# Performance work log

Hardware: AMD Instinct MI355X
Metric: run time of the kernel (lower is better)

## Reference

```python
import jax, jax.numpy as jnp
import numpy as np

N, IN_DIM, HID, EMB, PROJ = 12000, 256, 256, 128, 128
LN_EPS = 1e-5

def _layer_norm(h, gamma, beta):
    mu = jnp.mean(h, axis=-1, keepdims=True)
    var = jnp.mean(jnp.square(h - mu), axis=-1, keepdims=True)
    return (h - mu) * jax.lax.rsqrt(var + LN_EPS) * gamma + beta

def setup_inputs() -> dict:
    key = jax.random.key(0)
    ks = jax.random.split(key, 16)
    def lin(k, fan_in, fan_out):
        bound = 1.0 / np.sqrt(fan_in)
        kw, kb = jax.random.split(k)
        W = jax.random.uniform(kw, (fan_in, fan_out), jnp.float32, -bound, bound)
        b = jax.random.uniform(kb, (fan_out,), jnp.float32, -bound, bound)
        return W, b
    W1, b1 = lin(ks[0], IN_DIM, HID)
    W2, b2 = lin(ks[1], HID, HID)
    W3, b3 = lin(ks[2], HID, EMB)
    Wp1, bp1 = lin(ks[3], EMB, PROJ)
    Wp2, bp2 = lin(ks[4], PROJ, PROJ)
    x = jax.random.normal(ks[5], (N, IN_DIM), jnp.float32)
    # dense adjacency (row-stochastic-ish, scaled so aggregated values stay sane)
    adj = jax.random.uniform(ks[6], (N, N), jnp.float32) / N
    return {
        "x": x, "adj": adj,
        "W1": W1, "b1": b1, "g1": jnp.ones((HID,), jnp.float32), "be1": jnp.zeros((HID,), jnp.float32),
        "W2": W2, "b2": b2, "g2": jnp.ones((HID,), jnp.float32), "be2": jnp.zeros((HID,), jnp.float32),
        "W3": W3, "b3": b3,
        "Wp1": Wp1, "bp1": bp1, "Wp2": Wp2, "bp2": bp2,
    }

def reference(x, adj, W1, b1, g1, be1, W2, b2, g2, be2, W3, b3, Wp1, bp1, Wp2, bp2):
    # eval mode: dropout and dropout_adj are identity
    # layer 1: GCNConv_dense = A @ (x W + b); residual = x (in_dim == hidden_dim)
    h = adj @ (x @ W1 + b1)
    h = _layer_norm(h + x, g1, be1)
    h = jax.nn.relu(h)
    h_prev = h
    # layer 2
    h2 = adj @ (h @ W2 + b2)
    h2 = _layer_norm(h2 + h_prev, g2, be2)
    h2 = jax.nn.relu(h2)
    # final conv -> embedding (no norm/relu/residual)
    embedding = adj @ (h2 @ W3 + b3)
    # proj head: Linear -> ReLU -> Linear
    z = jax.nn.relu(embedding @ Wp1 + bp1) @ Wp2 + bp2
    return (z, embedding)
```

## Files before the change

### kernel.cpp

```cpp
#include <hip/hip_runtime.h>

typedef unsigned short u16;
typedef unsigned int u32;
typedef __attribute__((ext_vector_type(8))) short bf16x8;
typedef __attribute__((ext_vector_type(8))) u16 u16x8;
typedef __attribute__((ext_vector_type(4))) u16 u16x4;
typedef __attribute__((ext_vector_type(4))) float f32x4;

#define DEV static __device__ __forceinline__

DEV u16 f2bf(float f) {
    union { float f; u32 u; } v; v.f = f;
    u32 r = v.u + 0x7FFFu + ((v.u >> 16) & 1u);
    return (u16)(r >> 16);
}

DEV int swzc(int r, int c) { return c ^ ((r >> 1) & 3); }

DEV void gload_lds16(const void* g, void* l) {
    __builtin_amdgcn_global_load_lds((const __attribute__((address_space(1))) void*)g,
                                     (__attribute__((address_space(3))) void*)l, 16, 0, 0);
}

template<int BN, int MINW, bool AF32, bool BF32, bool DUMPA, int BIAS, bool RELU, bool OUTBF>
__global__ __launch_bounds__(256, MINW) void gemm_k(
    const void* __restrict__ Ap, const void* __restrict__ Bp, void* __restrict__ Cp,
    u16* __restrict__ Adump, const float* __restrict__ bias,
    int M, int N, int K, int lda, int ldb, int nRT, int nNT, int KCH)
{
    constexpr int BM = 64;
    constexpr int WN = BN / 4;
    constexpr int FI = 4;
    constexpr int FJ = WN / 16;
    constexpr int CPT = BN / 64;
    __shared__ u16 ldsA[2][BM * 32];
    __shared__ u16 ldsB[2][BN * 32];

    const int tid = threadIdx.x;
    int bid = blockIdx.x;
    const int rt = bid % nRT; bid /= nRT;
    const int nt = bid % nNT;
    const int s  = bid / nNT;
    const int m0 = rt * BM, n0 = nt * BN;
    const int kBeg = s * KCH;
    const int kEnd = (K < kBeg + KCH) ? K : (kBeg + KCH);
    const int nsteps = (kEnd - kBeg) >> 5;

    const int w = tid >> 6, l = tid & 63;
    const int wn = w * WN;
    const int lr = l & 15, lg = l >> 4;

    f32x4 acc[FI][FJ] = {};
    float aR[8], bR[8];

    auto aIssue = [&](int buf, int k0) {
        if constexpr (AF32) {
            const float* A = (const float*)Ap;
            int r = tid >> 2, q = tid & 3;
            int gm = m0 + r; gm = (gm < M) ? gm : (M - 1);
            const float4* src = (const float4*)(A + (size_t)gm * lda + k0 + q * 8);
            float4 v0 = src[0], v1 = src[1];
            aR[0]=v0.x; aR[1]=v0.y; aR[2]=v0.z; aR[3]=v0.w;
            aR[4]=v1.x; aR[5]=v1.y; aR[6]=v1.z; aR[7]=v1.w;
        } else {
            const u16* A = (const u16*)Ap;
            int r = tid >> 2, cs = tid & 3;
            int c = swzc(r, cs);
            int gm = m0 + r; gm = (gm < M) ? gm : (M - 1);
            gload_lds16(A + (size_t)gm * lda + k0 + c * 8, &ldsA[buf][tid * 8]);
        }
    };
    auto aCommit = [&](int buf, int k0) {
        if constexpr (AF32) {
            int r = tid >> 2, q = tid & 3;
            u16x8 pk;
            #pragma unroll
            for (int e = 0; e < 8; e++) pk[e] = f2bf(aR[e]);
            *(u16x8*)&ldsA[buf][r * 32 + swzc(r, q) * 8] = pk;
            if constexpr (DUMPA) {
                int gm = m0 + r;
                if (gm < M) *(u16x8*)(Adump + (size_t)gm * lda + k0 + q * 8) = pk;
            }
        }
    };
    auto bIssue = [&](int buf, int k0) {
        if constexpr (BF32) {
            const float* B = (const float*)Bp;
            int r = tid >> 2, q = tid & 3;
            int gn = n0 + r; gn = (gn < N) ? gn : (N - 1);
            const float4* src = (const float4*)(B + (size_t)gn * ldb + k0 + q * 8);
            float4 v0 = src[0], v1 = src[1];
            bR[0]=v0.x; bR[1]=v0.y; bR[2]=v0.z; bR[3]=v0.w;
            bR[4]=v1.x; bR[5]=v1.y; bR[6]=v1.z; bR[7]=v1.w;
        } else {
            const u16* B = (const u16*)Bp;
            #pragma unroll
            for (int u = 0; u < CPT; u++) {
                int slot = u * 256 + tid;
                int r = slot >> 2, cs = slot & 3;
                int c = swzc(r, cs);
                int gn = n0 + r; gn = (gn < N) ? gn : (N - 1);
                gload_lds16(B + (size_t)gn * ldb + k0 + c * 8, &ldsB[buf][slot * 8]);
            }
        }
    };
    auto bCommit = [&](int buf) {
        if constexpr (BF32) {
            int r = tid >> 2, q = tid & 3;
            u16x8 pk;
            #pragma unroll
            for (int e = 0; e < 8; e++) pk[e] = f2bf(bR[e]);
            *(u16x8*)&ldsB[buf][r * 32 + swzc(r, q) * 8] = pk;
        }
    };

    aIssue(0, kBeg); bIssue(0, kBeg);
    aCommit(0, kBeg); bCommit(0);
    __syncthreads();

    for (int t = 0; t < nsteps; t++) {
        const int k = kBeg + t * 32;
        const int cur = t & 1, nxt = cur ^ 1;
        if (t + 1 < nsteps) { aIssue(nxt, k + 32); bIssue(nxt, k + 32); }

        bf16x8 af[FI], bfr[FJ];
        #pragma unroll
        for (int i = 0; i < FI; i++) {
            int r = i * 16 + lr;
            af[i] = *(const bf16x8*)&ldsA[cur][r * 32 + swzc(r, lg) * 8];
        }
        #pragma unroll
        for (int j = 0; j < FJ; j++) {
            int r = wn + j * 16 + lr;
            bfr[j] = *(const bf16x8*)&ldsB[cur][r * 32 + swzc(r, lg) * 8];
        }
        #pragma unroll
        for (int i = 0; i < FI; i++)
            #pragma unroll
            for (int j = 0; j < FJ; j++)
                acc[i][j] = __builtin_amdgcn_mfma_f32_16x16x32_bf16(af[i], bfr[j], acc[i][j], 0, 0, 0);

        if (t + 1 < nsteps) { aCommit(nxt, k + 32); bCommit(nxt); }
        __syncthreads();
    }

    #pragma unroll
    for (int i = 0; i < FI; i++) {
        #pragma unroll
        for (int j = 0; j < FJ; j++) {
            #pragma unroll
            for (int e = 0; e < 4; e++) {
                int row = m0 + i * 16 + lg * 4 + e;
                int col = n0 + wn + j * 16 + lr;
                if (row < M && col < N) {
                    float v = acc[i][j][e];
                    if constexpr (BIAS == 1) v += bias[row];
                    if constexpr (BIAS == 2) v += bias[col];
                    if constexpr (RELU) v = fmaxf(v, 0.0f);
                    if constexpr (OUTBF) ((u16*)Cp)[(size_t)row * N + col] = f2bf(v);
                    else ((float*)Cp)[(size_t)s * M * N + (size_t)row * N + col] = v;
                }
            }
        }
    }
}

__global__ __launch_bounds__(256) void ln_k(
    const float* __restrict__ part, long pStride, int nPart,
    const float* __restrict__ resid, const float* __restrict__ gamma, const float* __restrict__ beta,
    u16* __restrict__ obf, float* __restrict__ of32, int M)
{
    const int w = threadIdx.x >> 6, l = threadIdx.x & 63;
    for (int row = blockIdx.x * 4 + w; row < M; row += gridDim.x * 4) {
        size_t base = (size_t)row * 256 + l * 4;
        float4 v = *(const float4*)(part + base);
        for (int s = 1; s < nPart; s++) {
            float4 u = *(const float4*)(part + (size_t)s * pStride + base);
            v.x += u.x; v.y += u.y; v.z += u.z; v.w += u.w;
        }
        float4 r = *(const float4*)(resid + base);
        v.x += r.x; v.y += r.y; v.z += r.z; v.w += r.w;
        float sum = v.x + v.y + v.z + v.w;
        float sq  = v.x*v.x + v.y*v.y + v.z*v.z + v.w*v.w;
        #pragma unroll
        for (int o = 32; o >= 1; o >>= 1) {
            sum += __shfl_xor(sum, o, 64);
            sq  += __shfl_xor(sq, o, 64);
        }
        float mu  = sum * (1.0f / 256.0f);
        float var = sq * (1.0f / 256.0f) - mu * mu;
        float sc  = rsqrtf(var + 1e-5f);
        int c = l * 4;
        float y0 = fmaxf((v.x - mu) * sc * gamma[c + 0] + beta[c + 0], 0.0f);
        float y1 = fmaxf((v.y - mu) * sc * gamma[c + 1] + beta[c + 1], 0.0f);
        float y2 = fmaxf((v.z - mu) * sc * gamma[c + 2] + beta[c + 2], 0.0f);
        float y3 = fmaxf((v.w - mu) * sc * gamma[c + 3] + beta[c + 3], 0.0f);
        u16x4 pk; pk[0] = f2bf(y0); pk[1] = f2bf(y1); pk[2] = f2bf(y2); pk[3] = f2bf(y3);
        *(u16x4*)(obf + base) = pk;
        if (of32) { float4 o4; o4.x = y0; o4.y = y1; o4.z = y2; o4.w = y3; *(float4*)(of32 + base) = o4; }
    }
}

__global__ __launch_bounds__(256) void sum_k(
    const float* __restrict__ p, long pStride, int nPart,
    float* __restrict__ of, u16* __restrict__ ob, int total4)
{
    int i = blockIdx.x * 256 + threadIdx.x;
    if (i >= total4) return;
    size_t b = (size_t)i * 4;
    float4 v = *(const float4*)(p + b);
    for (int s = 1; s < nPart; s++) {
        float4 u = *(const float4*)(p + (size_t)s * pStride + b);
        v.x += u.x; v.y += u.y; v.z += u.z; v.w += u.w;
    }
    *(float4*)(of + b) = v;
    u16x4 pk; pk[0] = f2bf(v.x); pk[1] = f2bf(v.y); pk[2] = f2bf(v.z); pk[3] = f2bf(v.w);
    *(u16x4*)(ob + b) = pk;
}

__global__ __launch_bounds__(256) void prep_k(
    const float* __restrict__ s0, const float* __restrict__ s1, const float* __restrict__ s2,
    const float* __restrict__ s3, const float* __restrict__ s4,
    u16* __restrict__ d0, u16* __restrict__ d1, u16* __restrict__ d2,
    u16* __restrict__ d3, u16* __restrict__ d4)
{
    int i = blockIdx.x * 256 + threadIdx.x;
    if (i < 65536) {
        int o = i >> 8, ii = i & 255; d0[i] = f2bf(s0[(size_t)ii * 256 + o]);
    } else if (i < 131072) {
        int j = i - 65536; int o = j >> 8, ii = j & 255; d1[j] = f2bf(s1[(size_t)ii * 256 + o]);
    } else if (i < 163840) {
        int j = i - 131072; int o = j >> 8, ii = j & 255; d2[j] = f2bf(s2[(size_t)ii * 128 + o]);
    } else if (i < 180224) {
        int j = i - 163840; int o = j >> 7, ii = j & 127; d3[j] = f2bf(s3[(size_t)ii * 128 + o]);
    } else if (i < 196608) {
        int j = i - 180224; int o = j >> 7, ii = j & 127; d4[j] = f2bf(s4[(size_t)ii * 128 + o]);
    }
}

extern "C" void kernel_launch(void* const* d_in, const int* in_sizes, int n_in,
                              void* d_out, int out_size, void* d_ws, size_t ws_size,
                              hipStream_t stream)
{
    if (n_in < 16) return;
    const int NN = 12000, DD = 256, EE = 128;
    const float* x   = (const float*)d_in[0];
    const float* adj = (const float*)d_in[1];
    const float* W1  = (const float*)d_in[2];
    const float* b1  = (const float*)d_in[3];
    const float* g1  = (const float*)d_in[4];
    const float* be1 = (const float*)d_in[5];
    const float* W2  = (const float*)d_in[6];
    const float* b2  = (const float*)d_in[7];
    const float* g2  = (const float*)d_in[8];
    const float* be2 = (const float*)d_in[9];
    const float* W3  = (const float*)d_in[10];
    const float* b3  = (const float*)d_in[11];
    const float* Wp1 = (const float*)d_in[12];
    const float* bp1 = (const float*)d_in[13];
    const float* Wp2 = (const float*)d_in[14];
    const float* bp2 = (const float*)d_in[15];
    float* zOut   = (float*)d_out;
    float* embOut = zOut + (size_t)NN * EE;

    char* ws = (char*)d_ws;
    size_t off = 0;
    auto alloc = [&](size_t bytes) -> void* {
        off = (off + 255) & ~(size_t)255;
        void* p = ws + off; off += bytes; return p;
    };

    const size_t adjElems = (size_t)NN * NN;
    bool cacheAdj = ws_size >= adjElems * 2 + 100000000ULL;
    u16* adjb = cacheAdj ? (u16*)alloc(adjElems * 2) : nullptr;

    u16* xW1t   = (u16*)alloc((size_t)DD * NN * 2);
    u16* hW2t   = (u16*)alloc((size_t)DD * NN * 2);
    u16* h2W3t  = (u16*)alloc((size_t)EE * NN * 2);
    u16* hbf    = (u16*)alloc((size_t)NN * DD * 2);
    float* hf32 = (float*)alloc((size_t)NN * DD * 4);
    u16* h2bf   = (u16*)alloc((size_t)NN * DD * 2);
    u16* embbf  = (u16*)alloc((size_t)NN * EE * 2);
    u16* p1bf   = (u16*)alloc((size_t)NN * EE * 2);
    u16* W1t    = (u16*)alloc(65536 * 2);
    u16* W2t    = (u16*)alloc(65536 * 2);
    u16* W3t    = (u16*)alloc(32768 * 2);
    u16* Wp1t   = (u16*)alloc(16384 * 2);
    u16* Wp2t   = (u16*)alloc(16384 * 2);

    int S = 4;
    if (off + (size_t)4 * NN * DD * 4 + 512 > ws_size) S = 1;
    float* part = (float*)alloc((size_t)S * NN * DD * 4);
    const int KCH = (S == 4) ? 3008 : 12032;

    prep_k<<<768, 256, 0, stream>>>(W1, W2, W3, Wp1, Wp2, W1t, W2t, W3t, Wp1t, Wp2t);

    gemm_k<64, 3, false, true, false, 1, false, true><<<4 * 188, 256, 0, stream>>>(
        W1t, x, xW1t, nullptr, b1, DD, NN, DD, DD, DD, 4, 188, DD);

    if (cacheAdj)
        gemm_k<256, 3, true, false, true, 0, false, false><<<188 * S, 256, 0, stream>>>(
            adj, xW1t, part, adjb, nullptr, NN, DD, NN, NN, NN, 188, 1, KCH);
    else
        gemm_k<256, 3, true, false, false, 0, false, false><<<188 * S, 256, 0, stream>>>(
            adj, xW1t, part, nullptr, nullptr, NN, DD, NN, NN, NN, 188, 1, KCH);

    ln_k<<<750, 256, 0, stream>>>(part, (long)NN * DD, S, x, g1, be1, hbf, hf32, NN);

    gemm_k<64, 4, false, false, false, 1, false, true><<<4 * 188, 256, 0, stream>>>(
        W2t, hbf, hW2t, nullptr, b2, DD, NN, DD, DD, DD, 4, 188, DD);

    if (cacheAdj)
        gemm_k<256, 4, false, false, false, 0, false, false><<<188 * S, 256, 0, stream>>>(
            adjb, hW2t, part, nullptr, nullptr, NN, DD, NN, NN, NN, 188, 1, KCH);
    else
        gemm_k<256, 3, true, false, false, 0, false, false><<<188 * S, 256, 0, stream>>>(
            adj, hW2t, part, nullptr, nullptr, NN, DD, NN, NN, NN, 188, 1, KCH);

    ln_k<<<750, 256, 0, stream>>>(part, (long)NN * DD, S, hf32, g2, be2, h2bf, nullptr, NN);

    gemm_k<64, 4, false, false, false, 1, false, true><<<2 * 188, 256, 0, stream>>>(
        W3t, h2bf, h2W3t, nullptr, b3, EE, NN, DD, DD, DD, 2, 188, DD);

    if (cacheAdj)
        gemm_k<128, 4, false, false, false, 0, false, false><<<188 * S, 256, 0, stream>>>(
            adjb, h2W3t, part, nullptr, nullptr, NN, EE, NN, NN, NN, 188, 1, KCH);
    else
        gemm_k<128, 3, true, false, false, 0, false, false><<<188 * S, 256, 0, stream>>>(
            adj, h2W3t, part, nullptr, nullptr, NN, EE, NN, NN, NN, 188, 1, KCH);

    sum_k<<<1500, 256, 0, stream>>>(part, (long)NN * EE, S, embOut, embbf, NN * EE / 4);

    gemm_k<128, 4, false, false, false, 2, true, true><<<188, 256, 0, stream>>>(
        embbf, Wp1t, p1bf, nullptr, bp1, NN, EE, EE, EE, EE, 188, 1, EE);

    gemm_k<128, 4, false, false, false, 2, false, false><<<188, 256, 0, stream>>>(
        p1bf, Wp2t, zOut, nullptr, bp2, NN, EE, EE, EE, EE, 188, 1, EE);
}
```

Before: 665.7 us.

## Replace LDS-tiled adjacency GEMMs with register-streaming kernel and XCD-aware block mapping

Adds a pstream_k kernel for the three big adj @ H products. It loads A and B fragments straight from global memory into registers with double buffering, bypassing LDS and __syncthreads, and converts fp32 adj to bf16 with the packed v_cvt_pk_bf16_f32 instruction. Blocks are remapped across the 8 XCDs, the last layer uses 8 K-splits with 2-wave blocks, and only wave 0 writes the bf16 adjacency dump. The intent is to cut LDS traffic and barrier stalls on the memory-bound adj streaming. The risks are redundant global loads of B across row tiles, and the fallback path when the S=1 workspace is too small has been removed.

```diff
diff --git a/kernel.cpp b/kernel.cpp
--- a/kernel.cpp
+++ b/kernel.cpp
@@ -5,6 +5,7 @@
 typedef __attribute__((ext_vector_type(8))) short bf16x8;
 typedef __attribute__((ext_vector_type(8))) u16 u16x8;
 typedef __attribute__((ext_vector_type(4))) u16 u16x4;
+typedef __attribute__((ext_vector_type(4))) u32 u32x4;
 typedef __attribute__((ext_vector_type(4))) float f32x4;
 
 #define DEV static __device__ __forceinline__
@@ -15,6 +16,12 @@
     return (u16)(r >> 16);
 }
 
+DEV u32 cvtpk(float lo, float hi) {
+    u32 r;
+    asm("v_cvt_pk_bf16_f32 %0, %1, %2" : "=v"(r) : "v"(lo), "v"(hi));
+    return r;
+}
+
 DEV int swzc(int r, int c) { return c ^ ((r >> 1) & 3); }
 
 DEV void gload_lds16(const void* g, void* l) {
@@ -22,10 +29,132 @@
                                      (__attribute__((address_space(3))) void*)l, 16, 0, 0);
 }
 
-template<int BN, int MINW, bool AF32, bool BF32, bool DUMPA, int BIAS, bool RELU, bool OUTBF>
+template<int WAVES, int MINW, bool AF32, bool DUMPA>
+__global__ __launch_bounds__(WAVES * 64, MINW) void pstream_k(
+    const void* __restrict__ Ap, const u16* __restrict__ Bt,
+    float* __restrict__ Cp, u16* __restrict__ Adump,
+    int M, int K, int lda, int ldb, int nRT, int KCH, int cpx)
+{
+    constexpr int NOUT = WAVES * 64;
+    const int tid = threadIdx.x;
+    int bid0 = blockIdx.x;
+    int bid = (bid0 & 7) * cpx + (bid0 >> 3);
+    const int rt = bid % nRT;
+    const int s  = bid / nRT;
+    const int m0 = rt * 64;
+    const int kBeg = s * KCH;
+    const int kEnd = (K < kBeg + KCH) ? K : (kBeg + KCH);
+    const int nsteps = (kEnd - kBeg) >> 5;
+
+    const int wv = tid >> 6, l = tid & 63;
+    const int wn = wv * 64;
+    const int lr = l & 15, lg = l >> 4;
+
+    int aoff[4], boff[4], arow[4];
+    #pragma unroll
+    for (int i = 0; i < 4; i++) {
+        int gm = m0 + i * 16 + lr; arow[i] = gm;
+        if (gm > M - 1) gm = M - 1;
+        aoff[i] = gm * lda + lg * 8;
+    }
+    #pragma unroll
+    for (int j = 0; j < 4; j++) boff[j] = (wn + j * 16 + lr) * ldb + lg * 8;
+
+    f32x4 acc[4][4] = {};
+    const u16* Ab = (const u16*)Ap;
+    const float* Af = (const float*)Ap;
+
+    bf16x8 a0[4], a1[4], b0[4], b1[4];
+    float4 r0[4][2], r1[4][2];
+
+    auto loadB = [&](bf16x8 (&bf)[4], int k) {
+        #pragma unroll
+        for (int j = 0; j < 4; j++)
+            bf[j] = *(const bf16x8*)(Bt + (size_t)k + boff[j]);
+    };
+    auto loadA16 = [&](bf16x8 (&af)[4], int k) {
+        #pragma unroll
+        for (int i = 0; i < 4; i++)
+            af[i] = *(const bf16x8*)(Ab + (size_t)k + aoff[i]);
+    };
+    auto loadA32 = [&](float4 (&raw)[4][2], int k) {
+        #pragma unroll
+        for (int i = 0; i < 4; i++) {
+            const float4* p = (const float4*)(Af + (size_t)k + aoff[i]);
+            raw[i][0] = p[0]; raw[i][1] = p[1];
+        }
+    };
+    auto cvtA = [&](float4 (&raw)[4][2], bf16x8 (&af)[4], int k) {
+        #pragma unroll
+        for (int i = 0; i < 4; i++) {
+            u32x4 pk;
+            pk[0] = cvtpk(raw[i][0].x, raw[i][0].y);
+            pk[1] = cvtpk(raw[i][0].z, raw[i][0].w);
+            pk[2] = cvtpk(raw[i][1].x, raw[i][1].y);
+            pk[3] = cvtpk(raw[i][1].z, raw[i][1].w);
+            af[i] = *(bf16x8*)&pk;
+            if constexpr (DUMPA) {
+                if (wv == 0 && arow[i] < M)
+                    *(u32x4*)(Adump + (size_t)k + aoff[i]) = pk;
+            }
+        }
+    };
+    auto mm = [&](bf16x8 (&af)[4], bf16x8 (&bf)[4]) {
+        #pragma unroll
+        for (int i = 0; i < 4; i++)
+            #pragma unroll
+            for (int j = 0; j < 4; j++)
+                acc[i][j] = __builtin_amdgcn_mfma_f32_16x16x32_bf16(af[i], bf[j], acc[i][j], 0, 0, 0);
+    };
+
+    if constexpr (!AF32) {
+        loadA16(a0, kBeg); loadB(b0, kBeg);
+        int t = 0;
+        for (; t + 2 <= nsteps; t += 2) {
+            int k1 = kBeg + (t + 1) * 32;
+            loadA16(a1, k1); loadB(b1, k1);
+            mm(a0, b0);
+            int k2 = kBeg + (t + 2) * 32;
+            if (t + 2 >= nsteps) k2 = kBeg + (nsteps - 1) * 32;
+            loadA16(a0, k2); loadB(b0, k2);
+            mm(a1, b1);
+        }
+        if (t < nsteps) mm(a0, b0);
+    } else {
+        loadA32(r0, kBeg); loadB(b0, kBeg);
+        int t = 0;
+        for (; t + 2 <= nsteps; t += 2) {
+            int kc = kBeg + t * 32;
+            int k1 = kc + 32;
+            loadA32(r1, k1); loadB(b1, k1);
+            cvtA(r0, a0, kc);
+            mm(a0, b0);
+            int k2 = kc + 64;
+            if (t + 2 >= nsteps) k2 = kBeg + (nsteps - 1) * 32;
+            loadA32(r0, k2); loadB(b0, k2);
+            cvtA(r1, a1, k1);
+            mm(a1, b1);
+        }
+        if (t < nsteps) { int kc = kBeg + t * 32; cvtA(r0, a0, kc); mm(a0, b0); }
+    }
+
+    float* Cbase = Cp + (size_t)s * M * NOUT;
+    #pragma unroll
+    for (int i = 0; i < 4; i++)
+        #pragma unroll
+        for (int j = 0; j < 4; j++)
+            #pragma unroll
+            for (int e = 0; e < 4; e++) {
+                int row = m0 + i * 16 + lg * 4 + e;
+                int col = wn + j * 16 + lr;
+                if (row < M) Cbase[(size_t)row * NOUT + col] = acc[i][j][e];
+            }
+}
+
+template<int BN, int MINW, bool AF32, bool BF32, int BIAS, bool RELU, bool OUTBF>
 __global__ __launch_bounds__(256, MINW) void gemm_k(
     const void* __restrict__ Ap, const void* __restrict__ Bp, void* __restrict__ Cp,
-    u16* __restrict__ Adump, const float* __restrict__ bias,
+    const float* __restrict__ bias,
     int M, int N, int K, int lda, int ldb, int nRT, int nNT, int KCH)
 {
     constexpr int BM = 64;
@@ -70,17 +199,13 @@
             gload_lds16(A + (size_t)gm * lda + k0 + c * 8, &ldsA[buf][tid * 8]);
         }
     };
-    auto aCommit = [&](int buf, int k0) {
+    auto aCommit = [&](int buf) {
         if constexpr (AF32) {
             int r = tid >> 2, q = tid & 3;
             u16x8 pk;
             #pragma unroll
             for (int e = 0; e < 8; e++) pk[e] = f2bf(aR[e]);
             *(u16x8*)&ldsA[buf][r * 32 + swzc(r, q) * 8] = pk;
-            if constexpr (DUMPA) {
-                int gm = m0 + r;
-                if (gm < M) *(u16x8*)(Adump + (size_t)gm * lda + k0 + q * 8) = pk;
-            }
         }
     };
     auto bIssue = [&](int buf, int k0) {
@@ -115,7 +240,7 @@
     };
 
     aIssue(0, kBeg); bIssue(0, kBeg);
-    aCommit(0, kBeg); bCommit(0);
+    aCommit(0); bCommit(0);
     __syncthreads();
 
     for (int t = 0; t < nsteps; t++) {
@@ -140,14 +265,14 @@
             for (int j = 0; j < FJ; j++)
                 acc[i][j] = __builtin_amdgcn_mfma_f32_16x16x32_bf16(af[i], bfr[j], acc[i][j], 0, 0, 0);
 
-        if (t + 1 < nsteps) { aCommit(nxt, k + 32); bCommit(nxt); }
+        if (t + 1 < nsteps) { aCommit(nxt); bCommit(nxt); }
         __syncthreads();
     }
 
     #pragma unroll
-    for (int i = 0; i < FI; i++) {
-        #pragma unroll
-        for (int j = 0; j < FJ; j++) {
+    for (int i = 0; i < FI; i++)
+        #pragma unroll
+        for (int j = 0; j < FJ; j++)
             #pragma unroll
             for (int e = 0; e < 4; e++) {
                 int row = m0 + i * 16 + lg * 4 + e;
@@ -161,8 +286,6 @@
                     else ((float*)Cp)[(size_t)s * M * N + (size_t)row * N + col] = v;
                 }
             }
-        }
-    }
 }
 
 __global__ __launch_bounds__(256) void ln_k(
@@ -288,52 +411,51 @@
     u16* Wp1t   = (u16*)alloc(16384 * 2);
     u16* Wp2t   = (u16*)alloc(16384 * 2);
 
-    int S = 4;
-    if (off + (size_t)4 * NN * DD * 4 + 512 > ws_size) S = 1;
-    float* part = (float*)alloc((size_t)S * NN * DD * 4);
-    const int KCH = (S == 4) ? 3008 : 12032;
+    float* part = (float*)alloc((size_t)4 * NN * DD * 4);
+    const int KCH4 = 3008;
+    const int KCH8 = 1504;
 
     prep_k<<<768, 256, 0, stream>>>(W1, W2, W3, Wp1, Wp2, W1t, W2t, W3t, Wp1t, Wp2t);
 
-    gemm_k<64, 3, false, true, false, 1, false, true><<<4 * 188, 256, 0, stream>>>(
-        W1t, x, xW1t, nullptr, b1, DD, NN, DD, DD, DD, 4, 188, DD);
+    gemm_k<64, 3, false, true, 1, false, true><<<4 * 188, 256, 0, stream>>>(
+        W1t, x, xW1t, b1, DD, NN, DD, DD, DD, 4, 188, DD);
 
     if (cacheAdj)
-        gemm_k<256, 3, true, false, true, 0, false, false><<<188 * S, 256, 0, stream>>>(
-            adj, xW1t, part, adjb, nullptr, NN, DD, NN, NN, NN, 188, 1, KCH);
+        pstream_k<4, 2, true, true><<<188 * 4, 256, 0, stream>>>(
+            adj, xW1t, part, adjb, NN, NN, NN, NN, 188, KCH4, 188 * 4 / 8);
     else
-        gemm_k<256, 3, true, false, false, 0, false, false><<<188 * S, 256, 0, stream>>>(
-            adj, xW1t, part, nullptr, nullptr, NN, DD, NN, NN, NN, 188, 1, KCH);
-
-    ln_k<<<750, 256, 0, stream>>>(part, (long)NN * DD, S, x, g1, be1, hbf, hf32, NN);
-
-    gemm_k<64, 4, false, false, false, 1, false, true><<<4 * 188, 256, 0, stream>>>(
-        W2t, hbf, hW2t, nullptr, b2, DD, NN, DD, DD, DD, 4, 188, DD);
+        pstream_k<4, 2, true, false><<<188 * 4, 256, 0, stream>>>(
+            adj, xW1t, part, nullptr, NN, NN, NN, NN, 188, KCH4, 188 * 4 / 8);
+
+    ln_k<<<750, 256, 0, stream>>>(part, (long)NN * DD, 4, x, g1, be1, hbf, hf32, NN);
+
+    gemm_k<64, 4, false, false, 1, false, true><<<4 * 188, 256, 0, stream>>>(
+        W2t, hbf, hW2t, b2, DD, NN, DD, DD, DD, 4, 188, DD);
 
     if (cacheAdj)
-        gemm_k<256, 4, false, false, false, 0, false, false><<<188 * S, 256, 0, stream>>>(
-            adjb, hW2t, part, nullptr, nullptr, NN, DD, NN, NN, NN, 188, 1, KCH);
+        pstream_k<4, 3, false, false><<<188 * 4, 256, 0, stream>>>(
+            adjb, hW2t, part, nullptr, NN, NN, NN, NN, 188, KCH4, 188 * 4 / 8);
     else
-        gemm_k<256, 3, true, false, false, 0, false, false><<<188 * S, 256, 0, stream>>>(
-            adj, hW2t, part, nullptr, nullptr, NN, DD, NN, NN, NN, 188, 1, KCH);
-
-    ln_k<<<750, 256, 0, stream>>>(part, (long)NN * DD, S, hf32, g2, be2, h2bf, nullptr, NN);
-
-    gemm_k<64, 4, false, false, false, 1, false, true><<<2 * 188, 256, 0, stream>>>(
-        W3t, h2bf, h2W3t, nullptr, b3, EE, NN, DD, DD, DD, 2, 188, DD);
+        pstream_k<4, 2, true, false><<<188 * 4, 256, 0, stream>>>(
+            adj, hW2t, part, nullptr, NN, NN, NN, NN, 188, KCH4, 188 * 4 / 8);
+
+    ln_k<<<750, 256, 0, stream>>>(part, (long)NN * DD, 4, hf32, g2, be2, h2bf, nullptr, NN);
+
+    gemm_k<64, 4, false, false, 1, false, true><<<2 * 188, 256, 0, stream>>>(
+        W3t, h2bf, h2W3t, b3, EE, NN, DD, DD, DD, 2, 188, DD);
 
     if (cacheAdj)
-        gemm_k<128, 4, false, false, false, 0, false, false><<<188 * S, 256, 0, stream>>>(
-            adjb, h2W3t, part, nullptr, nullptr, NN, EE, NN, NN, NN, 188, 1, KCH);
+        pstream_k<2, 3, false, false><<<188 * 8, 128, 0, stream>>>(
+            adjb, h2W3t, part, nullptr, NN, NN, NN, NN, 188, KCH8, 188 * 8 / 8);
     else
-        gemm_k<128, 3, true, false, false, 0, false, false><<<188 * S, 256, 0, stream>>>(
-            adj, h2W3t, part, nullptr, nullptr, NN, EE, NN, NN, NN, 188, 1, KCH);
-
-    sum_k<<<1500, 256, 0, stream>>>(part, (long)NN * EE, S, embOut, embbf, NN * EE / 4);
-
-    gemm_k<128, 4, false, false, false, 2, true, true><<<188, 256, 0, stream>>>(
-        embbf, Wp1t, p1bf, nullptr, bp1, NN, EE, EE, EE, EE, 188, 1, EE);
-
-    gemm_k<128, 4, false, false, false, 2, false, false><<<188, 256, 0, stream>>>(
-        p1bf, Wp2t, zOut, nullptr, bp2, NN, EE, EE, EE, EE, 188, 1, EE);
-}
+        pstream_k<2, 2, true, false><<<188 * 8, 128, 0, stream>>>(
+            adj, h2W3t, part, nullptr, NN, NN, NN, NN, 188, KCH8, 188 * 8 / 8);
+
+    sum_k<<<1500, 256, 0, stream>>>(part, (long)NN * EE, 8, embOut, embbf, NN * EE / 4);
+
+    gemm_k<128, 4, false, false, 2, true, true><<<188, 256, 0, stream>>>(
+        embbf, Wp1t, p1bf, bp1, NN, EE, EE, EE, EE, 188, 1, EE);
+
+    gemm_k<128, 4, false, false, 2, false, false><<<188, 256, 0, stream>>>(
+        p1bf, Wp2t, zOut, bp2, NN, EE, EE, EE, EE, 188, 1, EE);
+}
```

New measurement: 973.8 us. +46.3%, slower.

## Use BK=64 K-tiles with 8-way swizzle and packed bf16 convert for adj GEMMs

Applied to the files above, without the earlier changes.

Makes the GEMM K-tile size a template parameter and runs the three large adjacency GEMMs with BK=64 instead of 32. Each LDS stage therefore covers twice the K range, which halves the barriers per K and doubles the MFMA work between syncs. Alongside this, the fp32 A path uses nontemporal 64-byte loads, a hardware v_cvt_pk_bf16_f32 conversion, and nontemporal stores for the bf16 adj dump; K-tail handling is added. The larger LDS footprint lowers the occupancy hint to 2–3 waves, and the fallback for S=1 is removed.

```diff
diff --git a/kernel.cpp b/kernel.cpp
--- a/kernel.cpp
+++ b/kernel.cpp
@@ -5,6 +5,7 @@
 typedef __attribute__((ext_vector_type(8))) short bf16x8;
 typedef __attribute__((ext_vector_type(8))) u16 u16x8;
 typedef __attribute__((ext_vector_type(4))) u16 u16x4;
+typedef __attribute__((ext_vector_type(4))) u32 u32x4;
 typedef __attribute__((ext_vector_type(4))) float f32x4;
 
 #define DEV static __device__ __forceinline__
@@ -15,14 +16,18 @@
     return (u16)(r >> 16);
 }
 
-DEV int swzc(int r, int c) { return c ^ ((r >> 1) & 3); }
+DEV u32 cvtpk(float lo, float hi) {
+    u32 r;
+    asm("v_cvt_pk_bf16_f32 %0, %1, %2" : "=v"(r) : "v"(lo), "v"(hi));
+    return r;
+}
 
 DEV void gload_lds16(const void* g, void* l) {
     __builtin_amdgcn_global_load_lds((const __attribute__((address_space(1))) void*)g,
                                      (__attribute__((address_space(3))) void*)l, 16, 0, 0);
 }
 
-template<int BN, int MINW, bool AF32, bool BF32, bool DUMPA, int BIAS, bool RELU, bool OUTBF>
+template<int BN, int BK, int MINW, bool AF32, bool BF32, bool DUMPA, int BIAS, bool RELU, bool OUTBF>
 __global__ __launch_bounds__(256, MINW) void gemm_k(
     const void* __restrict__ Ap, const void* __restrict__ Bp, void* __restrict__ Cp,
     u16* __restrict__ Adump, const float* __restrict__ bias,
@@ -30,11 +35,12 @@
 {
     constexpr int BM = 64;
     constexpr int WN = BN / 4;
-    constexpr int FI = 4;
-    constexpr int FJ = WN / 16;
-    constexpr int CPT = BN / 64;
-    __shared__ u16 ldsA[2][BM * 32];
-    __shared__ u16 ldsB[2][BN * 32];
+    constexpr int FI = 4, FJ = WN / 16;
+    constexpr int CH = BK / 8;
+    constexpr int CPTA = (BM * CH) / 256;
+    constexpr int CPTB = (BN * CH) / 256;
+    __shared__ u16 ldsA[2][BM * BK];
+    __shared__ u16 ldsB[2][BN * BK];
 
     const int tid = threadIdx.x;
     int bid = blockIdx.x;
@@ -44,46 +50,63 @@
     const int m0 = rt * BM, n0 = nt * BN;
     const int kBeg = s * KCH;
     const int kEnd = (K < kBeg + KCH) ? K : (kBeg + KCH);
-    const int nsteps = (kEnd - kBeg) >> 5;
+    const int nsteps = (kEnd - kBeg + BK - 1) / BK;
 
     const int w = tid >> 6, l = tid & 63;
     const int wn = w * WN;
     const int lr = l & 15, lg = l >> 4;
 
     f32x4 acc[FI][FJ] = {};
-    float aR[8], bR[8];
-
-    auto aIssue = [&](int buf, int k0) {
+    f32x4 Rf[4];
+    float bR[8];
+
+    auto mask_of = [](int r) { return (BK == 64) ? (r & 7) : ((r >> 1) & 3); };
+
+    auto aIssueB = [&](int buf, int k0, int len) {
         if constexpr (AF32) {
-            const float* A = (const float*)Ap;
-            int r = tid >> 2, q = tid & 3;
+            int r = tid >> 2, qf = tid & 3;
             int gm = m0 + r; gm = (gm < M) ? gm : (M - 1);
-            const float4* src = (const float4*)(A + (size_t)gm * lda + k0 + q * 8);
-            float4 v0 = src[0], v1 = src[1];
-            aR[0]=v0.x; aR[1]=v0.y; aR[2]=v0.z; aR[3]=v0.w;
-            aR[4]=v1.x; aR[5]=v1.y; aR[6]=v1.z; aR[7]=v1.w;
+            int kc = (qf * 16 < len) ? (k0 + qf * 16) : k0;
+            const f32x4* p = (const f32x4*)((const float*)Ap + (size_t)gm * lda + kc);
+            Rf[0] = __builtin_nontemporal_load(p);
+            Rf[1] = __builtin_nontemporal_load(p + 1);
+            Rf[2] = __builtin_nontemporal_load(p + 2);
+            Rf[3] = __builtin_nontemporal_load(p + 3);
+            (void)buf;
         } else {
             const u16* A = (const u16*)Ap;
-            int r = tid >> 2, cs = tid & 3;
-            int c = swzc(r, cs);
-            int gm = m0 + r; gm = (gm < M) ? gm : (M - 1);
-            gload_lds16(A + (size_t)gm * lda + k0 + c * 8, &ldsA[buf][tid * 8]);
-        }
-    };
-    auto aCommit = [&](int buf, int k0) {
+            #pragma unroll
+            for (int u = 0; u < CPTA; u++) {
+                int slot = u * 256 + tid;
+                int r = slot / CH, c = slot % CH;
+                int q = c ^ mask_of(r);
+                int gm = m0 + r; gm = (gm < M) ? gm : (M - 1);
+                int kc = (q * 8 < len) ? (k0 + q * 8) : k0;
+                gload_lds16(A + (size_t)gm * lda + kc, &ldsA[buf][slot * 8]);
+            }
+        }
+    };
+    auto aCommit = [&](int buf, int k0, int len) {
         if constexpr (AF32) {
-            int r = tid >> 2, q = tid & 3;
-            u16x8 pk;
-            #pragma unroll
-            for (int e = 0; e < 8; e++) pk[e] = f2bf(aR[e]);
-            *(u16x8*)&ldsA[buf][r * 32 + swzc(r, q) * 8] = pk;
+            int r = tid >> 2, qf = tid & 3;
+            u32x4 pk0, pk1;
+            pk0[0] = cvtpk(Rf[0][0], Rf[0][1]); pk0[1] = cvtpk(Rf[0][2], Rf[0][3]);
+            pk0[2] = cvtpk(Rf[1][0], Rf[1][1]); pk0[3] = cvtpk(Rf[1][2], Rf[1][3]);
+            pk1[0] = cvtpk(Rf[2][0], Rf[2][1]); pk1[1] = cvtpk(Rf[2][2], Rf[2][3]);
+            pk1[2] = cvtpk(Rf[3][0], Rf[3][1]); pk1[3] = cvtpk(Rf[3][2], Rf[3][3]);
+            int mk = mask_of(r);
+            *(u32x4*)&ldsA[buf][r * BK + ((qf * 2) ^ mk) * 8]     = pk0;
+            *(u32x4*)&ldsA[buf][r * BK + ((qf * 2 + 1) ^ mk) * 8] = pk1;
             if constexpr (DUMPA) {
-                int gm = m0 + r;
-                if (gm < M) *(u16x8*)(Adump + (size_t)gm * lda + k0 + q * 8) = pk;
-            }
-        }
-    };
-    auto bIssue = [&](int buf, int k0) {
+                if (m0 + r < M && qf * 16 < len) {
+                    u16* d = Adump + (size_t)(m0 + r) * lda + k0 + qf * 16;
+                    __builtin_nontemporal_store(pk0, (u32x4*)d);
+                    __builtin_nontemporal_store(pk1, (u32x4*)(d + 8));
+                }
+            }
+        }
+    };
+    auto bIssue = [&](int buf, int k0, int len) {
         if constexpr (BF32) {
             const float* B = (const float*)Bp;
             int r = tid >> 2, q = tid & 3;
@@ -92,15 +115,17 @@
             float4 v0 = src[0], v1 = src[1];
             bR[0]=v0.x; bR[1]=v0.y; bR[2]=v0.z; bR[3]=v0.w;
             bR[4]=v1.x; bR[5]=v1.y; bR[6]=v1.z; bR[7]=v1.w;
+            (void)buf; (void)len;
         } else {
             const u16* B = (const u16*)Bp;
             #pragma unroll
-            for (int u = 0; u < CPT; u++) {
+            for (int u = 0; u < CPTB; u++) {
                 int slot = u * 256 + tid;
-                int r = slot >> 2, cs = slot & 3;
-                int c = swzc(r, cs);
+                int r = slot / CH, c = slot % CH;
+                int q = c ^ mask_of(r);
                 int gn = n0 + r; gn = (gn < N) ? gn : (N - 1);
-                gload_lds16(B + (size_t)gn * ldb + k0 + c * 8, &ldsB[buf][slot * 8]);
+                int kc = (q * 8 < len) ? (k0 + q * 8) : k0;
+                gload_lds16(B + (size_t)gn * ldb + kc, &ldsB[buf][slot * 8]);
             }
         }
     };
@@ -110,44 +135,54 @@
             u16x8 pk;
             #pragma unroll
             for (int e = 0; e < 8; e++) pk[e] = f2bf(bR[e]);
-            *(u16x8*)&ldsB[buf][r * 32 + swzc(r, q) * 8] = pk;
-        }
-    };
-
-    aIssue(0, kBeg); bIssue(0, kBeg);
-    aCommit(0, kBeg); bCommit(0);
+            *(u16x8*)&ldsB[buf][r * BK + (q ^ mask_of(r)) * 8] = pk;
+        }
+    };
+
+    int len0 = kEnd - kBeg; if (len0 > BK) len0 = BK;
+    aIssueB(0, kBeg, len0); bIssue(0, kBeg, len0);
+    aCommit(0, kBeg, len0); bCommit(0);
     __syncthreads();
 
     for (int t = 0; t < nsteps; t++) {
-        const int k = kBeg + t * 32;
+        const int k0 = kBeg + t * BK;
+        int lt = kEnd - k0; if (lt > BK) lt = BK;
         const int cur = t & 1, nxt = cur ^ 1;
-        if (t + 1 < nsteps) { aIssue(nxt, k + 32); bIssue(nxt, k + 32); }
-
-        bf16x8 af[FI], bfr[FJ];
+        const bool hasNext = (t + 1 < nsteps);
+        int kn = k0 + BK;
+        int ln = kEnd - kn; if (ln > BK) ln = BK;
+        if (hasNext) { aIssueB(nxt, kn, ln); bIssue(nxt, kn, ln); }
+
         #pragma unroll
-        for (int i = 0; i < FI; i++) {
-            int r = i * 16 + lr;
-            af[i] = *(const bf16x8*)&ldsA[cur][r * 32 + swzc(r, lg) * 8];
-        }
-        #pragma unroll
-        for (int j = 0; j < FJ; j++) {
-            int r = wn + j * 16 + lr;
-            bfr[j] = *(const bf16x8*)&ldsB[cur][r * 32 + swzc(r, lg) * 8];
-        }
-        #pragma unroll
-        for (int i = 0; i < FI; i++)
-            #pragma unroll
-            for (int j = 0; j < FJ; j++)
-                acc[i][j] = __builtin_amdgcn_mfma_f32_16x16x32_bf16(af[i], bfr[j], acc[i][j], 0, 0, 0);
-
-        if (t + 1 < nsteps) { aCommit(nxt, k + 32); bCommit(nxt); }
+        for (int kk = 0; kk < BK / 32; kk++) {
+            if (kk * 32 < lt) {
+                bf16x8 af[FI], bfr[FJ];
+                #pragma unroll
+                for (int i = 0; i < FI; i++) {
+                    int r = i * 16 + lr;
+                    af[i] = *(const bf16x8*)&ldsA[cur][r * BK + ((kk * 4 + lg) ^ mask_of(r)) * 8];
+                }
+                #pragma unroll
+                for (int j = 0; j < FJ; j++) {
+                    int r = wn + j * 16 + lr;
+                    bfr[j] = *(const bf16x8*)&ldsB[cur][r * BK + ((kk * 4 + lg) ^ mask_of(r)) * 8];
+                }
+                #pragma unroll
+                for (int i = 0; i < FI; i++)
+                    #pragma unroll
+                    for (int j = 0; j < FJ; j++)
+                        acc[i][j] = __builtin_amdgcn_mfma_f32_16x16x32_bf16(af[i], bfr[j], acc[i][j], 0, 0, 0);
+            }
+        }
+
+        if (hasNext) { aCommit(nxt, kn, ln); bCommit(nxt); }
         __syncthreads();
     }
 
     #pragma unroll
-    for (int i = 0; i < FI; i++) {
+    for (int i = 0; i < FI; i++)
         #pragma unroll
-        for (int j = 0; j < FJ; j++) {
+        for (int j = 0; j < FJ; j++)
             #pragma unroll
             for (int e = 0; e < 4; e++) {
                 int row = m0 + i * 16 + lg * 4 + e;
@@ -161,8 +196,6 @@
                     else ((float*)Cp)[(size_t)s * M * N + (size_t)row * N + col] = v;
                 }
             }
-        }
-    }
 }
 
 __global__ __launch_bounds__(256) void ln_k(
@@ -288,52 +321,51 @@
     u16* Wp1t   = (u16*)alloc(16384 * 2);
     u16* Wp2t   = (u16*)alloc(16384 * 2);
 
-    int S = 4;
-    if (off + (size_t)4 * NN * DD * 4 + 512 > ws_size) S = 1;
+    const int S = 4;
     float* part = (float*)alloc((size_t)S * NN * DD * 4);
-    const int KCH = (S == 4) ? 3008 : 12032;
+    const int KCH = 3008;
 
     prep_k<<<768, 256, 0, stream>>>(W1, W2, W3, Wp1, Wp2, W1t, W2t, W3t, Wp1t, Wp2t);
 
-    gemm_k<64, 3, false, true, false, 1, false, true><<<4 * 188, 256, 0, stream>>>(
+    gemm_k<64, 32, 3, false, true, false, 1, false, true><<<4 * 188, 256, 0, stream>>>(
         W1t, x, xW1t, nullptr, b1, DD, NN, DD, DD, DD, 4, 188, DD);
 
     if (cacheAdj)
-        gemm_k<256, 3, true, false, true, 0, false, false><<<188 * S, 256, 0, stream>>>(
+        gemm_k<256, 64, 2, true, false, true, 0, false, false><<<188 * S, 256, 0, stream>>>(
             adj, xW1t, part, adjb, nullptr, NN, DD, NN, NN, NN, 188, 1, KCH);
     else
-        gemm_k<256, 3, true, false, false, 0, false, false><<<188 * S, 256, 0, stream>>>(
+        gemm_k<256, 64, 2, true, false, false, 0, false, false><<<188 * S, 256, 0, stream>>>(
             adj, xW1t, part, nullptr, nullptr, NN, DD, NN, NN, NN, 188, 1, KCH);
 
     ln_k<<<750, 256, 0, stream>>>(part, (long)NN * DD, S, x, g1, be1, hbf, hf32, NN);
 
-    gemm_k<64, 4, false, false, false, 1, false, true><<<4 * 188, 256, 0, stream>>>(
+    gemm_k<64, 32, 4, false, false, false, 1, false, true><<<4 * 188, 256, 0, stream>>>(
         W2t, hbf, hW2t, nullptr, b2, DD, NN, DD, DD, DD, 4, 188, DD);
 
     if (cacheAdj)
-        gemm_k<256, 4, false, false, false, 0, false, false><<<188 * S, 256, 0, stream>>>(
+        gemm_k<256, 64, 2, false, false, false, 0, false, false><<<188 * S, 256, 0, stream>>>(
             adjb, hW2t, part, nullptr, nullptr, NN, DD, NN, NN, NN, 188, 1, KCH);
     else
-        gemm_k<256, 3, true, false, false, 0, false, false><<<188 * S, 256, 0, stream>>>(
+        gemm_k<256, 64, 2, true, false, false, 0, false, false><<<188 * S, 256, 0, stream>>>(
             adj, hW2t, part, nullptr, nullptr, NN, DD, NN, NN, NN, 188, 1, KCH);
 
     ln_k<<<750, 256, 0, stream>>>(part, (long)NN * DD, S, hf32, g2, be2, h2bf, nullptr, NN);
 
-    gemm_k<64, 4, false, false, false, 1, false, true><<<2 * 188, 256, 0, stream>>>(
+    gemm_k<64, 32, 4, false, false, false, 1, false, true><<<2 * 188, 256, 0, stream>>>(
         W3t, h2bf, h2W3t, nullptr, b3, EE, NN, DD, DD, DD, 2, 188, DD);
 
     if (cacheAdj)
-        gemm_k<128, 4, false, false, false, 0, false, false><<<188 * S, 256, 0, stream>>>(
+        gemm_k<128, 64, 3, false, false, false, 0, false, false><<<188 * S, 256, 0, stream>>>(
             adjb, h2W3t, part, nullptr, nullptr, NN, EE, NN, NN, NN, 188, 1, KCH);
     else
-        gemm_k<128, 3, true, false, false, 0, false, false><<<188 * S, 256, 0, stream>>>(
+        gemm_k<128, 64, 3, true, false, false, 0, false, false><<<188 * S, 256, 0, stream>>>(
             adj, h2W3t, part, nullptr, nullptr, NN, EE, NN, NN, NN, 188, 1, KCH);
 
     sum_k<<<1500, 256, 0, stream>>>(part, (long)NN * EE, S, embOut, embbf, NN * EE / 4);
 
-    gemm_k<128, 4, false, false, false, 2, true, true><<<188, 256, 0, stream>>>(
+    gemm_k<128, 32, 4, false, false, false, 2, true, true><<<188, 256, 0, stream>>>(
         embbf, Wp1t, p1bf, nullptr, bp1, NN, EE, EE, EE, EE, 188, 1, EE);
 
-    gemm_k<128, 4, false, false, false, 2, false, false><<<188, 256, 0, stream>>>(
+    gemm_k<128, 32, 4, false, false, false, 2, false, false><<<188, 256, 0, stream>>>(
         p1bf, Wp2t, zOut, nullptr, bp2, NN, EE, EE, EE, EE, 188, 1, EE);
 }
```

Measured after the change: 789.5 us. 18.6% more time.

## Add triple-buffered bf16 adjacency GEMM kernel with explicit vmcnt waits

Applied to the files above, without the earlier changes.

Adds a specialised padj_k kernel for the second and third adjacency GEMMs on the cached bf16 adjacency. It uses three LDS buffers with loads issued two steps ahead, precomputed global offsets, and explicit s_waitcnt vmcnt plus s_barrier in place of __syncthreads, so global-to-LDS loads overlap MFMA work. The extra LDS buffer and the lower occupancy hint for the BN=256 variant trade occupancy for deeper prefetch. The split-K fallback to S=1 when workspace is short is also removed.

```diff
diff --git a/kernel.cpp b/kernel.cpp
--- a/kernel.cpp
+++ b/kernel.cpp
@@ -20,6 +20,102 @@
 DEV void gload_lds16(const void* g, void* l) {
     __builtin_amdgcn_global_load_lds((const __attribute__((address_space(1))) void*)g,
                                      (__attribute__((address_space(3))) void*)l, 16, 0, 0);
+}
+
+template<int N> DEV void waitcnt_vm() {
+    if constexpr (N == 0) asm volatile("s_waitcnt vmcnt(0) lgkmcnt(0)" ::: "memory");
+    else if constexpr (N == 3) asm volatile("s_waitcnt vmcnt(3) lgkmcnt(0)" ::: "memory");
+    else if constexpr (N == 5) asm volatile("s_waitcnt vmcnt(5) lgkmcnt(0)" ::: "memory");
+}
+
+template<int BN, int MINW, int NLOADS>
+__global__ __launch_bounds__(256, MINW) void padj_k(
+    const u16* __restrict__ Ab, const u16* __restrict__ Bt, float* __restrict__ Cp,
+    int M, int K, int lda, int ldb, int nRT, int KCH)
+{
+    constexpr int BM = 64, BK = 32;
+    constexpr int WN = BN / 4, FJ = WN / 16;
+    constexpr int CPTB = BN / 64;
+    __shared__ u16 ldsA[3][BM * BK];
+    __shared__ u16 ldsB[3][BN * BK];
+
+    const int tid = threadIdx.x;
+    const int bid = blockIdx.x;
+    const int rt = bid % nRT;
+    const int s  = bid / nRT;
+    const int m0 = rt * BM;
+    const int kBeg = s * KCH;
+    const int kEnd = (K < kBeg + KCH) ? K : (kBeg + KCH);
+    const int nsteps = (kEnd - kBeg) >> 5;
+
+    const int w = tid >> 6, l = tid & 63;
+    const int wn = w * WN;
+    const int lr = l & 15, lg = l >> 4;
+
+    const int ar = tid >> 2, ac = tid & 3;
+    int gmA = m0 + ar; if (gmA > M - 1) gmA = M - 1;
+    const size_t aoff = (size_t)gmA * lda + swzc(ar, ac) * 8;
+    size_t boff[CPTB];
+    #pragma unroll
+    for (int u = 0; u < CPTB; u++) {
+        int slot = u * 256 + tid;
+        int r = slot >> 2, c = slot & 3;
+        boff[u] = (size_t)r * ldb + swzc(r, c) * 8;
+    }
+
+    f32x4 acc[4][FJ] = {};
+
+    auto stage = [&](int buf, int k0) {
+        gload_lds16(Ab + aoff + k0, &ldsA[buf][tid * 8]);
+        #pragma unroll
+        for (int u = 0; u < CPTB; u++)
+            gload_lds16(Bt + boff[u] + k0, &ldsB[buf][(u * 256 + tid) * 8]);
+    };
+
+    stage(0, kBeg);
+    if (nsteps > 1) stage(1, kBeg + 32);
+    if (nsteps > 1) waitcnt_vm<NLOADS>(); else waitcnt_vm<0>();
+    __builtin_amdgcn_s_barrier();
+    __builtin_amdgcn_sched_barrier(0);
+
+    for (int t = 0; t < nsteps; t++) {
+        const int cur = t % 3;
+        const bool deep = (t + 2 < nsteps);
+        if (deep) stage((t + 2) % 3, kBeg + (t + 2) * 32);
+
+        bf16x8 af[4], bf[FJ];
+        #pragma unroll
+        for (int i = 0; i < 4; i++) {
+            int r = i * 16 + lr;
+            af[i] = *(const bf16x8*)&ldsA[cur][r * BK + swzc(r, lg) * 8];
+        }
+        #pragma unroll
+        for (int j = 0; j < FJ; j++) {
+            int r = wn + j * 16 + lr;
+            bf[j] = *(const bf16x8*)&ldsB[cur][r * BK + swzc(r, lg) * 8];
+        }
+        #pragma unroll
+        for (int i = 0; i < 4; i++)
+            #pragma unroll
+            for (int j = 0; j < FJ; j++)
+                acc[i][j] = __builtin_amdgcn_mfma_f32_16x16x32_bf16(af[i], bf[j], acc[i][j], 0, 0, 0);
+
+        if (deep) waitcnt_vm<NLOADS>(); else waitcnt_vm<0>();
+        __builtin_amdgcn_s_barrier();
+        __builtin_amdgcn_sched_barrier(0);
+    }
+
+    float* Cbase = Cp + (size_t)s * M * BN;
+    #pragma unroll
+    for (int i = 0; i < 4; i++)
+        #pragma unroll
+        for (int j = 0; j < FJ; j++)
+            #pragma unroll
+            for (int e = 0; e < 4; e++) {
+                int row = m0 + i * 16 + lg * 4 + e;
+                int col = wn + j * 16 + lr;
+                if (row < M) Cbase[(size_t)row * BN + col] = acc[i][j][e];
+            }
 }
 
 template<int BN, int MINW, bool AF32, bool BF32, bool DUMPA, int BIAS, bool RELU, bool OUTBF>
@@ -62,6 +158,7 @@
             float4 v0 = src[0], v1 = src[1];
             aR[0]=v0.x; aR[1]=v0.y; aR[2]=v0.z; aR[3]=v0.w;
             aR[4]=v1.x; aR[5]=v1.y; aR[6]=v1.z; aR[7]=v1.w;
+            (void)buf;
         } else {
             const u16* A = (const u16*)Ap;
             int r = tid >> 2, cs = tid & 3;
@@ -92,6 +189,7 @@
             float4 v0 = src[0], v1 = src[1];
             bR[0]=v0.x; bR[1]=v0.y; bR[2]=v0.z; bR[3]=v0.w;
             bR[4]=v1.x; bR[5]=v1.y; bR[6]=v1.z; bR[7]=v1.w;
+            (void)buf;
         } else {
             const u16* B = (const u16*)Bp;
             #pragma unroll
@@ -145,9 +243,9 @@
     }
 
     #pragma unroll
-    for (int i = 0; i < FI; i++) {
-        #pragma unroll
-        for (int j = 0; j < FJ; j++) {
+    for (int i = 0; i < FI; i++)
+        #pragma unroll
+        for (int j = 0; j < FJ; j++)
             #pragma unroll
             for (int e = 0; e < 4; e++) {
                 int row = m0 + i * 16 + lg * 4 + e;
@@ -161,8 +259,6 @@
                     else ((float*)Cp)[(size_t)s * M * N + (size_t)row * N + col] = v;
                 }
             }
-        }
-    }
 }
 
 __global__ __launch_bounds__(256) void ln_k(
@@ -288,10 +384,9 @@
     u16* Wp1t   = (u16*)alloc(16384 * 2);
     u16* Wp2t   = (u16*)alloc(16384 * 2);
 
-    int S = 4;
-    if (off + (size_t)4 * NN * DD * 4 + 512 > ws_size) S = 1;
+    const int S = 4;
     float* part = (float*)alloc((size_t)S * NN * DD * 4);
-    const int KCH = (S == 4) ? 3008 : 12032;
+    const int KCH = 3008;
 
     prep_k<<<768, 256, 0, stream>>>(W1, W2, W3, Wp1, Wp2, W1t, W2t, W3t, Wp1t, Wp2t);
 
@@ -311,8 +406,8 @@
         W2t, hbf, hW2t, nullptr, b2, DD, NN, DD, DD, DD, 4, 188, DD);
 
     if (cacheAdj)
-        gemm_k<256, 4, false, false, false, 0, false, false><<<188 * S, 256, 0, stream>>>(
-            adjb, hW2t, part, nullptr, nullptr, NN, DD, NN, NN, NN, 188, 1, KCH);
+        padj_k<256, 2, 5><<<188 * S, 256, 0, stream>>>(
+            adjb, hW2t, part, NN, NN, NN, NN, 188, KCH);
     else
         gemm_k<256, 3, true, false, false, 0, false, false><<<188 * S, 256, 0, stream>>>(
             adj, hW2t, part, nullptr, nullptr, NN, DD, NN, NN, NN, 188, 1, KCH);
@@ -323,8 +418,8 @@
         W3t, h2bf, h2W3t, nullptr, b3, EE, NN, DD, DD, DD, 2, 188, DD);
 
     if (cacheAdj)
-        gemm_k<128, 4, false, false, false, 0, false, false><<<188 * S, 256, 0, stream>>>(
-            adjb, h2W3t, part, nullptr, nullptr, NN, EE, NN, NN, NN, 188, 1, KCH);
+        padj_k<128, 4, 3><<<188 * S, 256, 0, stream>>>(
+            adjb, h2W3t, part, NN, NN, NN, NN, 188, KCH);
     else
         gemm_k<128, 3, true, false, false, 0, false, false><<<188 * S, 256, 0, stream>>>(
             adj, h2W3t, part, nullptr, nullptr, NN, EE, NN, NN, NN, 188, 1, KCH);
```

New measurement: 701.4 us. 5.4% more time.
